# Kernel tuning notes

Measured on AMD Instinct MI355X. Metric: run time of the kernel, lower is better.

The kernel has to match this reference:

```python
import jax, jax.numpy as jnp
import numpy as np

N_NODES = 100000
N_EDGES = 3200000
IN_CH = 128
HID = 64
OUT_CH = 2
BN_EPS = 1e-5


def setup_inputs() -> dict:
    key = jax.random.key(0)
    ks = jax.random.split(key, 16)
    def glorot(k, shape):
        fan_in, fan_out = shape[0], shape[1]
        lim = jnp.sqrt(6.0 / (fan_in + fan_out))
        return jax.random.uniform(k, shape, jnp.float32, -lim, lim)
    inp = {
        "x": jax.random.normal(ks[0], (N_NODES, IN_CH), jnp.float32),
        "edge_index": jax.random.randint(ks[1], (2, N_EDGES), 0, N_NODES, jnp.int64),
        # input projection + input BN
        "Wp": glorot(ks[2], (IN_CH, HID)),
        "bp": jnp.zeros((HID,), jnp.float32),
        "g_in": jnp.ones((HID,), jnp.float32),
        "b_in": jnp.zeros((HID,), jnp.float32),
        # SAGEConv layer 0: lin_l (aggr, with bias) + lin_r (self, no bias)
        "Wl0": glorot(ks[3], (HID, HID)),
        "bl0": jnp.zeros((HID,), jnp.float32),
        "Wr0": glorot(ks[4], (HID, HID)),
        "g0": jnp.ones((HID,), jnp.float32),
        "b0": jnp.zeros((HID,), jnp.float32),
        # SAGEConv layer 1
        "Wl1": glorot(ks[5], (HID, HID)),
        "bl1": jnp.zeros((HID,), jnp.float32),
        "Wr1": glorot(ks[6], (HID, HID)),
        "g1": jnp.ones((HID,), jnp.float32),
        "b1": jnp.zeros((HID,), jnp.float32),
        # output head
        "Wo": glorot(ks[7], (HID, OUT_CH)),
        "bo": jnp.zeros((OUT_CH,), jnp.float32),
    }
    return inp


def _bn(h, g, b):
    # training-mode batchnorm over node dim (biased variance, as torch)
    m = h.mean(axis=0)
    v = h.var(axis=0)
    return g * (h - m) * jax.lax.rsqrt(v + BN_EPS) + b


def _sage_conv(h, src, dst, Wl, bl, Wr):
    # mean aggregation of source features at destination nodes
    msg = h[src]                                              # [E, HID]
    summed = jax.ops.segment_sum(msg, dst, num_segments=N_NODES)
    cnt = jax.ops.segment_sum(jnp.ones((src.shape[0],), h.dtype), dst,
                              num_segments=N_NODES)
    aggr = summed / jnp.maximum(cnt, 1.0)[:, None]
    return aggr @ Wl + bl + h @ Wr


def reference(x, edge_index, Wp, bp, g_in, b_in,
              Wl0, bl0, Wr0, g0, b0,
              Wl1, bl1, Wr1, g1, b1,
              Wo, bo):
    src, dst = edge_index[0], edge_index[1]
    h = jax.nn.relu(_bn(x @ Wp + bp, g_in, b_in))   # dropout: eval no-op
    h_prev = h
    # layer 0 (i=0: no residual)
    h_new = jax.nn.relu(_bn(_sage_conv(h, src, dst, Wl0, bl0, Wr0), g0, b0))
    h_prev, h = h, h_new
    # layer 1 (i=1: residual with h_prev)
    h_new = jax.nn.relu(_bn(_sage_conv(h, src, dst, Wl1, bl1, Wr1), g1, b1))
    h_new = h_new + h_prev
    h = h_new
    return h @ Wo + bo
```

## Files before the change

kernel.cpp:

```cpp
#include <hip/hip_runtime.h>
#include <hip/hip_bf16.h>

#define NN 100000
#define NE 3200000
#define IC 128
#define HD 64
#define BN_EPS 1e-5f
#define NBUK 196
#define MSB 16

__device__ __forceinline__ float bf2f(unsigned short u) {
  return __uint_as_float(((unsigned)u) << 16);
}
__device__ __forceinline__ unsigned int f2bf(float f) {
  unsigned int u = __float_as_uint(f);
  return (u + 0x7FFFu + ((u >> 16) & 1u)) >> 16;
}

__global__ __launch_bounds__(256) void k_gemm_in(
    const float* __restrict__ x, const float* __restrict__ Wp,
    const float* __restrict__ bp, float* __restrict__ pre,
    float* __restrict__ stats) {
  __shared__ float sW[IC * HD];
  __shared__ float sX[64 * 130];
  __shared__ float ssS[1024], ssQ[1024];
  int tid = threadIdx.x;
  for (int i = tid; i < IC * HD / 4; i += 256)
    *(float4*)&sW[i * 4] = *(const float4*)&Wp[i * 4];
  int cg = tid & 15, rg = tid >> 4;
  int c0 = cg * 4;
  float4 bpc = *(const float4*)&bp[c0];
  float S[4] = {0.f, 0.f, 0.f, 0.f}, Q[4] = {0.f, 0.f, 0.f, 0.f};
  const int NT = (NN + 63) / 64;
  for (int t = blockIdx.x; t < NT; t += gridDim.x) {
    int row0 = t * 64;
    __syncthreads();
    for (int i = tid; i < 64 * IC / 4; i += 256) {
      int r = i >> 5, k4 = i & 31;
      int grow = row0 + r;
      if (grow >= NN) grow = NN - 1;
      *(float4*)&sX[r * 130 + k4 * 4] =
          *(const float4*)&x[(size_t)grow * IC + k4 * 4];
    }
    __syncthreads();
    float acc[4][4];
#pragma unroll
    for (int r = 0; r < 4; ++r)
#pragma unroll
      for (int c = 0; c < 4; ++c) acc[r][c] = ((const float*)&bpc)[c];
    for (int kg = 0; kg < IC; kg += 4) {
      float4 xr[4], wv[4];
#pragma unroll
      for (int r = 0; r < 4; ++r)
        xr[r] = *(const float4*)&sX[(rg * 4 + r) * 130 + kg];
#pragma unroll
      for (int j = 0; j < 4; ++j)
        wv[j] = *(const float4*)&sW[(kg + j) * HD + c0];
#pragma unroll
      for (int j = 0; j < 4; ++j)
#pragma unroll
        for (int r = 0; r < 4; ++r) {
          float xv = ((const float*)&xr[r])[j];
          acc[r][0] = fmaf(xv, ((const float*)&wv[j])[0], acc[r][0]);
          acc[r][1] = fmaf(xv, ((const float*)&wv[j])[1], acc[r][1]);
          acc[r][2] = fmaf(xv, ((const float*)&wv[j])[2], acc[r][2]);
          acc[r][3] = fmaf(xv, ((const float*)&wv[j])[3], acc[r][3]);
        }
    }
#pragma unroll
    for (int r = 0; r < 4; ++r) {
      int row = row0 + rg * 4 + r;
      if (row < NN) {
        *(float4*)&pre[(size_t)row * HD + c0] = *(float4*)&acc[r][0];
#pragma unroll
        for (int c = 0; c < 4; ++c) {
          S[c] += acc[r][c];
          Q[c] = fmaf(acc[r][c], acc[r][c], Q[c]);
        }
      }
    }
  }
#pragma unroll
  for (int c = 0; c < 4; ++c) {
    ssS[tid * 4 + c] = S[c];
    ssQ[tid * 4 + c] = Q[c];
  }
  __syncthreads();
  if (tid < 64) {
    int cgr = tid >> 2, cc = tid & 3;
    float Ts = 0.f, Tq = 0.f;
#pragma unroll
    for (int m = 0; m < 16; ++m) {
      Ts += ssS[(m * 16 + cgr) * 4 + cc];
      Tq += ssQ[(m * 16 + cgr) * 4 + cc];
    }
    atomicAdd(&stats[tid], Ts);
    atomicAdd(&stats[64 + tid], Tq);
  }
}

__global__ __launch_bounds__(256) void k_bn_relu(
    const float* __restrict__ pre, const float* __restrict__ stats,
    const float* __restrict__ g, const float* __restrict__ b,
    __hip_bfloat16* __restrict__ out16) {
  size_t i = (size_t)blockIdx.x * 256 + threadIdx.x;
  int c = threadIdx.x & 63;
  const float invN = 1.0f / NN;
  float m = stats[c] * invN;
  float v = stats[64 + c] * invN - m * m;
  float sc = g[c] * rsqrtf(v + BN_EPS);
  float val = (pre[i] - m) * sc + b[c];
  out16[i] = __float2bfloat16(fmaxf(val, 0.f));
}

__global__ __launch_bounds__(256) void k_bhist(
    const int* __restrict__ dst, unsigned int* __restrict__ bcnt) {
  __shared__ unsigned int h[NBUK];
  for (int i = threadIdx.x; i < NBUK; i += 256) h[i] = 0u;
  __syncthreads();
  int i0 = blockIdx.x * 256 + threadIdx.x;
  int stride = gridDim.x * 256;
  for (int e = i0; e < NE; e += stride)
    atomicAdd(&h[((unsigned)dst[e]) >> 9], 1u);
  __syncthreads();
  for (int i = threadIdx.x; i < NBUK; i += 256)
    if (h[i]) atomicAdd(&bcnt[i], h[i]);
}

__global__ __launch_bounds__(256) void k_bscan(
    const unsigned int* __restrict__ bcnt, unsigned int* __restrict__ gstart,
    unsigned int* __restrict__ gcur) {
  __shared__ unsigned int s[256];
  int t = threadIdx.x;
  unsigned int my = (t < NBUK) ? bcnt[t] : 0u;
  s[t] = my;
  __syncthreads();
  for (int off = 1; off < 256; off <<= 1) {
    unsigned int v = (t >= off) ? s[t - off] : 0u;
    __syncthreads();
    s[t] += v;
    __syncthreads();
  }
  if (t < NBUK) {
    gstart[t] = s[t] - my;
    gcur[t] = s[t] - my;
  }
  if (t == NBUK - 1) gstart[NBUK] = s[t];
}

__global__ __launch_bounds__(256) void k_msplit(
    const int* __restrict__ src, const int* __restrict__ dst,
    unsigned int* __restrict__ gcur, unsigned int* __restrict__ staging) {
  __shared__ unsigned int hist[NBUK];
  __shared__ unsigned int gbase[NBUK];
  int tid = threadIdx.x;
  for (int i = tid; i < NBUK; i += 256) hist[i] = 0u;
  __syncthreads();
  int e0 = blockIdx.x * (256 * MSB);
  unsigned int pk[MSB], rk[MSB], bk[MSB];
#pragma unroll
  for (int i = 0; i < MSB; ++i) {
    int e = e0 + i * 256 + tid;
    if (e < NE) {
      int d = dst[e];
      unsigned int b = (unsigned int)(d >> 9);
      rk[i] = atomicAdd(&hist[b], 1u);
      pk[i] = (unsigned int)src[e] | ((unsigned int)(d & 511) << 17);
      bk[i] = b;
    } else {
      bk[i] = 0xFFFFFFFFu;
    }
  }
  __syncthreads();
  for (int i = tid; i < NBUK; i += 256)
    if (hist[i]) gbase[i] = atomicAdd(&gcur[i], hist[i]);
  __syncthreads();
#pragma unroll
  for (int i = 0; i < MSB; ++i)
    if (bk[i] != 0xFFFFFFFFu) staging[gbase[bk[i]] + rk[i]] = pk[i];
}

__global__ __launch_bounds__(512) void k_bucket_sort(
    const unsigned int* __restrict__ staging,
    const unsigned int* __restrict__ gstart, unsigned int* __restrict__ nstart,
    unsigned int* __restrict__ srcoff) {
  __shared__ unsigned int hist[512];
  __shared__ unsigned int sc[512];
  __shared__ unsigned int cur[512];
  int b = blockIdx.x, t = threadIdx.x;
  hist[t] = 0u;
  __syncthreads();
  int lo = (int)gstart[b], hi = (int)gstart[b + 1];
  for (int e = lo + t; e < hi; e += 512)
    atomicAdd(&hist[staging[e] >> 17], 1u);
  __syncthreads();
  unsigned int my = hist[t];
  sc[t] = my;
  __syncthreads();
  for (int off = 1; off < 512; off <<= 1) {
    unsigned int v = (t >= off) ? sc[t - off] : 0u;
    __syncthreads();
    sc[t] += v;
    __syncthreads();
  }
  unsigned int st = (unsigned int)lo + sc[t] - my;
  cur[t] = st;
  int node = b * 512 + t;
  if (node < NN) {
    nstart[node] = st;
    if (node == NN - 1) nstart[NN] = st + my;
  }
  __syncthreads();
  for (int e = lo + t; e < hi; e += 512) {
    unsigned int u = staging[e];
    unsigned int pos = atomicAdd(&cur[u >> 17], 1u);
    srcoff[pos] = (u & 0x1FFFFu) << 7;
  }
}

__global__ __launch_bounds__(256) void k_aggr_sorted(
    const unsigned int* __restrict__ srcoff,
    const unsigned int* __restrict__ nstart,
    const unsigned short* __restrict__ h16,
    unsigned short* __restrict__ a16) {
  int lane = threadIdx.x & 63;
  int n = (int)((blockIdx.x * 256 + threadIdx.x) >> 6);
  if (n >= NN) return;
  int g = lane >> 3;
  int q = lane & 7;
  int e0 = (int)nstart[n];
  int e1 = (int)nstart[n + 1];
  const char* hbase = (const char*)h16 + q * 16;
  float a0 = 0.f, a1 = 0.f, a2 = 0.f, a3 = 0.f;
  float a4 = 0.f, a5 = 0.f, a6 = 0.f, a7 = 0.f;
  float b0 = 0.f, b1 = 0.f, b2 = 0.f, b3 = 0.f;
  float b4 = 0.f, b5 = 0.f, b6 = 0.f, b7 = 0.f;
  int e = e0 + g;
  for (; e + 8 < e1; e += 16) {
    unsigned int o0 = srcoff[e];
    unsigned int o1 = srcoff[e + 8];
    uint4 u0 = *(const uint4*)(hbase + o0);
    uint4 u1 = *(const uint4*)(hbase + o1);
    a0 += __uint_as_float(u0.x << 16);
    a1 += __uint_as_float(u0.x & 0xFFFF0000u);
    a2 += __uint_as_float(u0.y << 16);
    a3 += __uint_as_float(u0.y & 0xFFFF0000u);
    a4 += __uint_as_float(u0.z << 16);
    a5 += __uint_as_float(u0.z & 0xFFFF0000u);
    a6 += __uint_as_float(u0.w << 16);
    a7 += __uint_as_float(u0.w & 0xFFFF0000u);
    b0 += __uint_as_float(u1.x << 16);
    b1 += __uint_as_float(u1.x & 0xFFFF0000u);
    b2 += __uint_as_float(u1.y << 16);
    b3 += __uint_as_float(u1.y & 0xFFFF0000u);
    b4 += __uint_as_float(u1.z << 16);
    b5 += __uint_as_float(u1.z & 0xFFFF0000u);
    b6 += __uint_as_float(u1.w << 16);
    b7 += __uint_as_float(u1.w & 0xFFFF0000u);
  }
  if (e < e1) {
    unsigned int o0 = srcoff[e];
    uint4 u0 = *(const uint4*)(hbase + o0);
    a0 += __uint_as_float(u0.x << 16);
    a1 += __uint_as_float(u0.x & 0xFFFF0000u);
    a2 += __uint_as_float(u0.y << 16);
    a3 += __uint_as_float(u0.y & 0xFFFF0000u);
    a4 += __uint_as_float(u0.z << 16);
    a5 += __uint_as_float(u0.z & 0xFFFF0000u);
    a6 += __uint_as_float(u0.w << 16);
    a7 += __uint_as_float(u0.w & 0xFFFF0000u);
  }
  a0 += b0; a1 += b1; a2 += b2; a3 += b3;
  a4 += b4; a5 += b5; a6 += b6; a7 += b7;
#pragma unroll
  for (int off = 8; off <= 32; off <<= 1) {
    a0 += __shfl_xor(a0, off);
    a1 += __shfl_xor(a1, off);
    a2 += __shfl_xor(a2, off);
    a3 += __shfl_xor(a3, off);
    a4 += __shfl_xor(a4, off);
    a5 += __shfl_xor(a5, off);
    a6 += __shfl_xor(a6, off);
    a7 += __shfl_xor(a7, off);
  }
  if (g == 0) {
    float cntf = (float)(e1 - e0);
    float inv = (cntf > 0.f) ? 1.0f / cntf : 0.f;
    uint4 o;
    o.x = f2bf(a0 * inv) | (f2bf(a1 * inv) << 16);
    o.y = f2bf(a2 * inv) | (f2bf(a3 * inv) << 16);
    o.z = f2bf(a4 * inv) | (f2bf(a5 * inv) << 16);
    o.w = f2bf(a6 * inv) | (f2bf(a7 * inv) << 16);
    *(uint4*)((char*)a16 + (size_t)n * 128 + q * 16) = o;
  }
}

__global__ __launch_bounds__(256) void k_combine(
    const unsigned short* __restrict__ a16,
    const unsigned short* __restrict__ h16, const float* __restrict__ Wl,
    const float* __restrict__ bl, const float* __restrict__ Wr,
    float* __restrict__ pre, float* __restrict__ stats) {
  __shared__ float sWl[HD * HD], sWr[HD * HD];
  __shared__ float sA[64 * 66], sH[64 * 66];
  __shared__ float ssS[1024], ssQ[1024];
  int tid = threadIdx.x;
  for (int i = tid; i < HD * HD / 4; i += 256) {
    *(float4*)&sWl[i * 4] = *(const float4*)&Wl[i * 4];
    *(float4*)&sWr[i * 4] = *(const float4*)&Wr[i * 4];
  }
  int cg = tid & 15, rg = tid >> 4;
  int c0 = cg * 4;
  float4 blc = *(const float4*)&bl[c0];
  float S[4] = {0.f, 0.f, 0.f, 0.f}, Q[4] = {0.f, 0.f, 0.f, 0.f};
  const int NT = (NN + 63) / 64;
  for (int t = blockIdx.x; t < NT; t += gridDim.x) {
    int row0 = t * 64;
    __syncthreads();
    for (int i = tid; i < 1024; i += 256) {
      int r = i >> 4, k4 = i & 15;
      int grow = row0 + r;
      if (grow >= NN) grow = NN - 1;
      uint2 au = *(const uint2*)&a16[(size_t)grow * HD + k4 * 4];
      float* dA = &sA[r * 66 + k4 * 4];
      dA[0] = bf2f((unsigned short)(au.x & 0xFFFFu));
      dA[1] = bf2f((unsigned short)(au.x >> 16));
      dA[2] = bf2f((unsigned short)(au.y & 0xFFFFu));
      dA[3] = bf2f((unsigned short)(au.y >> 16));
      uint2 hu = *(const uint2*)&h16[(size_t)grow * HD + k4 * 4];
      float* dH = &sH[r * 66 + k4 * 4];
      dH[0] = bf2f((unsigned short)(hu.x & 0xFFFFu));
      dH[1] = bf2f((unsigned short)(hu.x >> 16));
      dH[2] = bf2f((unsigned short)(hu.y & 0xFFFFu));
      dH[3] = bf2f((unsigned short)(hu.y >> 16));
    }
    __syncthreads();
    float acc[4][4];
#pragma unroll
    for (int r = 0; r < 4; ++r)
#pragma unroll
      for (int c = 0; c < 4; ++c) acc[r][c] = ((const float*)&blc)[c];
    for (int kg = 0; kg < HD; kg += 4) {
      float4 ar[4], hr[4], wlv[4], wrv[4];
#pragma unroll
      for (int r = 0; r < 4; ++r) {
        ar[r] = *(const float4*)&sA[(rg * 4 + r) * 66 + kg];
        hr[r] = *(const float4*)&sH[(rg * 4 + r) * 66 + kg];
      }
#pragma unroll
      for (int j = 0; j < 4; ++j) {
        wlv[j] = *(const float4*)&sWl[(kg + j) * HD + c0];
        wrv[j] = *(const float4*)&sWr[(kg + j) * HD + c0];
      }
#pragma unroll
      for (int j = 0; j < 4; ++j)
#pragma unroll
        for (int r = 0; r < 4; ++r) {
          float av = ((const float*)&ar[r])[j];
          float hv = ((const float*)&hr[r])[j];
#pragma unroll
          for (int c = 0; c < 4; ++c) {
            acc[r][c] = fmaf(av, ((const float*)&wlv[j])[c], acc[r][c]);
            acc[r][c] = fmaf(hv, ((const float*)&wrv[j])[c], acc[r][c]);
          }
        }
    }
#pragma unroll
    for (int r = 0; r < 4; ++r) {
      int row = row0 + rg * 4 + r;
      if (row < NN) {
        *(float4*)&pre[(size_t)row * HD + c0] = *(float4*)&acc[r][0];
#pragma unroll
        for (int c = 0; c < 4; ++c) {
          S[c] += acc[r][c];
          Q[c] = fmaf(acc[r][c], acc[r][c], Q[c]);
        }
      }
    }
  }
#pragma unroll
  for (int c = 0; c < 4; ++c) {
    ssS[tid * 4 + c] = S[c];
    ssQ[tid * 4 + c] = Q[c];
  }
  __syncthreads();
  if (tid < 64) {
    int cgr = tid >> 2, cc = tid & 3;
    float Ts = 0.f, Tq = 0.f;
#pragma unroll
    for (int m = 0; m < 16; ++m) {
      Ts += ssS[(m * 16 + cgr) * 4 + cc];
      Tq += ssQ[(m * 16 + cgr) * 4 + cc];
    }
    atomicAdd(&stats[tid], Ts);
    atomicAdd(&stats[64 + tid], Tq);
  }
}

__global__ __launch_bounds__(256) void k_bn_relu_head(
    const float* __restrict__ pre, const float* __restrict__ stats,
    const float* __restrict__ g, const float* __restrict__ b,
    const unsigned short* __restrict__ resid16, const float* __restrict__ Wo,
    const float* __restrict__ bo, float* __restrict__ out) {
  int lane = threadIdx.x & 63;
  int wid = (int)((blockIdx.x * blockDim.x + threadIdx.x) >> 6);
  int nw = (int)((gridDim.x * blockDim.x) >> 6);
  const float invN = 1.0f / NN;
  float m = stats[lane] * invN;
  float v = stats[64 + lane] * invN - m * m;
  float sc = g[lane] * rsqrtf(v + BN_EPS);
  float bb = b[lane];
  float w0 = Wo[lane * 2], w1 = Wo[lane * 2 + 1];
  float b0 = bo[0], b1 = bo[1];
  for (int row = wid; row < NN; row += nw) {
    size_t i = (size_t)row * HD + lane;
    float val = (pre[i] - m) * sc + bb;
    val = fmaxf(val, 0.f) + bf2f(resid16[i]);
    float a0 = val * w0, a1 = val * w1;
#pragma unroll
    for (int off = 32; off > 0; off >>= 1) {
      a0 += __shfl_down(a0, off);
      a1 += __shfl_down(a1, off);
    }
    if (lane == 0) {
      out[(size_t)row * 2] = a0 + b0;
      out[(size_t)row * 2 + 1] = a1 + b1;
    }
  }
}

extern "C" void kernel_launch(void* const* d_in, const int* in_sizes, int n_in,
                              void* d_out, int out_size, void* d_ws,
                              size_t ws_size, hipStream_t stream) {
  const float* x = (const float*)d_in[0];
  const int* ei = (const int*)d_in[1];
  const float* Wp = (const float*)d_in[2];
  const float* bp = (const float*)d_in[3];
  const float* g_in = (const float*)d_in[4];
  const float* b_in = (const float*)d_in[5];
  const float* Wl0 = (const float*)d_in[6];
  const float* bl0 = (const float*)d_in[7];
  const float* Wr0 = (const float*)d_in[8];
  const float* g0 = (const float*)d_in[9];
  const float* b0 = (const float*)d_in[10];
  const float* Wl1 = (const float*)d_in[11];
  const float* bl1 = (const float*)d_in[12];
  const float* Wr1 = (const float*)d_in[13];
  const float* g1 = (const float*)d_in[14];
  const float* b1 = (const float*)d_in[15];
  const float* Wo = (const float*)d_in[16];
  const float* bo = (const float*)d_in[17];
  float* out = (float*)d_out;

  const int* src = ei;
  const int* dst = ei + NE;

  float* ws = (float*)d_ws;
  float* pre = ws;
  __hip_bfloat16* h0b = (__hip_bfloat16*)(ws + (size_t)NN * HD);
  __hip_bfloat16* h1b = h0b + (size_t)NN * HD;
  unsigned short* a16 = (unsigned short*)(h1b + (size_t)NN * HD);
  unsigned int* staging = (unsigned int*)(a16 + (size_t)NN * HD);
  unsigned int* srcoff = staging + NE;
  unsigned int* nstart = srcoff + NE;
  unsigned int* bcnt = nstart + NN + 1;
  unsigned int* gstart = bcnt + NBUK;
  unsigned int* gcur = gstart + NBUK + 1;
  float* stats0 = (float*)(gcur + NBUK);
  float* stats1 = stats0 + 128;
  float* stats2 = stats1 + 128;

  const int ELEM_BLOCKS = (NN * HD) / 256;
  const int AGGR_BLOCKS = 25000;
  const int MS_BLOCKS = (NE + 256 * MSB - 1) / (256 * MSB);

  hipMemsetAsync(stats0, 0, 3 * 128 * sizeof(float), stream);
  hipMemsetAsync(bcnt, 0, NBUK * sizeof(unsigned int), stream);

  k_gemm_in<<<512, 256, 0, stream>>>(x, Wp, bp, pre, stats0);
  k_bn_relu<<<ELEM_BLOCKS, 256, 0, stream>>>(pre, stats0, g_in, b_in, h0b);

  k_bhist<<<1024, 256, 0, stream>>>(dst, bcnt);
  k_bscan<<<1, 256, 0, stream>>>(bcnt, gstart, gcur);
  k_msplit<<<MS_BLOCKS, 256, 0, stream>>>(src, dst, gcur, staging);
  k_bucket_sort<<<NBUK, 512, 0, stream>>>(staging, gstart, nstart, srcoff);

  k_aggr_sorted<<<AGGR_BLOCKS, 256, 0, stream>>>(
      srcoff, nstart, (const unsigned short*)h0b, a16);
  k_combine<<<512, 256, 0, stream>>>(a16, (const unsigned short*)h0b, Wl0,
                                     bl0, Wr0, pre, stats1);
  k_bn_relu<<<ELEM_BLOCKS, 256, 0, stream>>>(pre, stats1, g0, b0, h1b);

  k_aggr_sorted<<<AGGR_BLOCKS, 256, 0, stream>>>(
      srcoff, nstart, (const unsigned short*)h1b, a16);
  k_combine<<<512, 256, 0, stream>>>(a16, (const unsigned short*)h1b, Wl1,
                                     bl1, Wr1, pre, stats2);
  k_bn_relu_head<<<1024, 256, 0, stream>>>(pre, stats2, g1, b1,
                                           (const unsigned short*)h0b, Wo, bo,
                                           out);
}
```

Baseline: 399.8 us.

## Store pre-BN activations and staged tiles in bf16, shuffle-reduce BN stats

Pre-batchnorm activations are now written and read as packed bf16 instead of fp32, which halves the traffic between the GEMM kernels and the BN kernels. The input x tile and the aggregation and self tiles are staged in LDS as packed bf16 and unpacked in registers, cutting shared-memory footprint so more blocks can be resident. BN statistics are reduced with wave shuffles instead of a large LDS array, k_bn_relu processes four elements per thread, and the GEMM grids grow from 512 to 768 blocks. This adds rounding error to x and to the pre-BN values, and costs extra unpack work in the inner loops.

```diff
diff --git a/kernel.cpp b/kernel.cpp
--- a/kernel.cpp
+++ b/kernel.cpp
@@ -16,14 +16,17 @@
   unsigned int u = __float_as_uint(f);
   return (u + 0x7FFFu + ((u >> 16) & 1u)) >> 16;
 }
+__device__ __forceinline__ unsigned int pack2(float a, float b) {
+  return f2bf(a) | (f2bf(b) << 16);
+}
 
 __global__ __launch_bounds__(256) void k_gemm_in(
     const float* __restrict__ x, const float* __restrict__ Wp,
-    const float* __restrict__ bp, float* __restrict__ pre,
+    const float* __restrict__ bp, unsigned int* __restrict__ pre16,
     float* __restrict__ stats) {
   __shared__ float sW[IC * HD];
-  __shared__ float sX[64 * 130];
-  __shared__ float ssS[1024], ssQ[1024];
+  __shared__ unsigned int sXu[64 * 68];
+  __shared__ float sStS[256], sStQ[256];
   int tid = threadIdx.x;
   for (int i = tid; i < IC * HD / 4; i += 256)
     *(float4*)&sW[i * 4] = *(const float4*)&Wp[i * 4];
@@ -35,12 +38,19 @@
   for (int t = blockIdx.x; t < NT; t += gridDim.x) {
     int row0 = t * 64;
     __syncthreads();
-    for (int i = tid; i < 64 * IC / 4; i += 256) {
-      int r = i >> 5, k4 = i & 31;
+    for (int i = tid; i < 1024; i += 256) {
+      int r = i >> 4, k8 = i & 15;
       int grow = row0 + r;
       if (grow >= NN) grow = NN - 1;
-      *(float4*)&sX[r * 130 + k4 * 4] =
-          *(const float4*)&x[(size_t)grow * IC + k4 * 4];
+      const float* xs = &x[(size_t)grow * IC + k8 * 8];
+      float4 f0 = *(const float4*)xs;
+      float4 f1 = *(const float4*)(xs + 4);
+      uint4 p;
+      p.x = pack2(f0.x, f0.y);
+      p.y = pack2(f0.z, f0.w);
+      p.z = pack2(f1.x, f1.y);
+      p.w = pack2(f1.z, f1.w);
+      *(uint4*)&sXu[r * 68 + k8 * 4] = p;
     }
     __syncthreads();
     float acc[4][4];
@@ -49,29 +59,37 @@
 #pragma unroll
       for (int c = 0; c < 4; ++c) acc[r][c] = ((const float*)&bpc)[c];
     for (int kg = 0; kg < IC; kg += 4) {
-      float4 xr[4], wv[4];
+      uint2 xu[4];
+      float4 wv[4];
 #pragma unroll
       for (int r = 0; r < 4; ++r)
-        xr[r] = *(const float4*)&sX[(rg * 4 + r) * 130 + kg];
+        xu[r] = *(const uint2*)&sXu[(rg * 4 + r) * 68 + (kg >> 1)];
 #pragma unroll
       for (int j = 0; j < 4; ++j)
         wv[j] = *(const float4*)&sW[(kg + j) * HD + c0];
 #pragma unroll
-      for (int j = 0; j < 4; ++j)
-#pragma unroll
-        for (int r = 0; r < 4; ++r) {
-          float xv = ((const float*)&xr[r])[j];
-          acc[r][0] = fmaf(xv, ((const float*)&wv[j])[0], acc[r][0]);
-          acc[r][1] = fmaf(xv, ((const float*)&wv[j])[1], acc[r][1]);
-          acc[r][2] = fmaf(xv, ((const float*)&wv[j])[2], acc[r][2]);
-          acc[r][3] = fmaf(xv, ((const float*)&wv[j])[3], acc[r][3]);
+      for (int r = 0; r < 4; ++r) {
+        float xv[4];
+        xv[0] = __uint_as_float(xu[r].x << 16);
+        xv[1] = __uint_as_float(xu[r].x & 0xFFFF0000u);
+        xv[2] = __uint_as_float(xu[r].y << 16);
+        xv[3] = __uint_as_float(xu[r].y & 0xFFFF0000u);
+#pragma unroll
+        for (int j = 0; j < 4; ++j) {
+#pragma unroll
+          for (int c = 0; c < 4; ++c)
+            acc[r][c] = fmaf(xv[j], ((const float*)&wv[j])[c], acc[r][c]);
         }
+      }
     }
 #pragma unroll
     for (int r = 0; r < 4; ++r) {
       int row = row0 + rg * 4 + r;
       if (row < NN) {
-        *(float4*)&pre[(size_t)row * HD + c0] = *(float4*)&acc[r][0];
+        uint2 o;
+        o.x = pack2(acc[r][0], acc[r][1]);
+        o.y = pack2(acc[r][2], acc[r][3]);
+        *(uint2*)&pre16[(size_t)row * 32 + cg * 2] = o;
 #pragma unroll
         for (int c = 0; c < 4; ++c) {
           S[c] += acc[r][c];
@@ -82,35 +100,52 @@
   }
 #pragma unroll
   for (int c = 0; c < 4; ++c) {
-    ssS[tid * 4 + c] = S[c];
-    ssQ[tid * 4 + c] = Q[c];
+    S[c] += __shfl_xor(S[c], 16);
+    S[c] += __shfl_xor(S[c], 32);
+    Q[c] += __shfl_xor(Q[c], 16);
+    Q[c] += __shfl_xor(Q[c], 32);
+  }
+  int wave = tid >> 6, lane = tid & 63;
+  if (lane < 16) {
+#pragma unroll
+    for (int c = 0; c < 4; ++c) {
+      sStS[wave * 64 + lane * 4 + c] = S[c];
+      sStQ[wave * 64 + lane * 4 + c] = Q[c];
+    }
   }
   __syncthreads();
   if (tid < 64) {
-    int cgr = tid >> 2, cc = tid & 3;
-    float Ts = 0.f, Tq = 0.f;
-#pragma unroll
-    for (int m = 0; m < 16; ++m) {
-      Ts += ssS[(m * 16 + cgr) * 4 + cc];
-      Tq += ssQ[(m * 16 + cgr) * 4 + cc];
-    }
+    float Ts = sStS[tid] + sStS[64 + tid] + sStS[128 + tid] + sStS[192 + tid];
+    float Tq = sStQ[tid] + sStQ[64 + tid] + sStQ[128 + tid] + sStQ[192 + tid];
     atomicAdd(&stats[tid], Ts);
     atomicAdd(&stats[64 + tid], Tq);
   }
 }
 
 __global__ __launch_bounds__(256) void k_bn_relu(
-    const float* __restrict__ pre, const float* __restrict__ stats,
+    const unsigned int* __restrict__ pre16, const float* __restrict__ stats,
     const float* __restrict__ g, const float* __restrict__ b,
-    __hip_bfloat16* __restrict__ out16) {
+    unsigned int* __restrict__ h16u) {
   size_t i = (size_t)blockIdx.x * 256 + threadIdx.x;
-  int c = threadIdx.x & 63;
+  int c0 = ((int)(i & 15)) * 4;
   const float invN = 1.0f / NN;
-  float m = stats[c] * invN;
-  float v = stats[64 + c] * invN - m * m;
-  float sc = g[c] * rsqrtf(v + BN_EPS);
-  float val = (pre[i] - m) * sc + b[c];
-  out16[i] = __float2bfloat16(fmaxf(val, 0.f));
+  uint2 p = *(const uint2*)&pre16[i * 2];
+  float v[4];
+  v[0] = __uint_as_float(p.x << 16);
+  v[1] = __uint_as_float(p.x & 0xFFFF0000u);
+  v[2] = __uint_as_float(p.y << 16);
+  v[3] = __uint_as_float(p.y & 0xFFFF0000u);
+#pragma unroll
+  for (int c = 0; c < 4; ++c) {
+    float m = stats[c0 + c] * invN;
+    float var = stats[64 + c0 + c] * invN - m * m;
+    float sc = g[c0 + c] * rsqrtf(var + BN_EPS);
+    v[c] = fmaxf((v[c] - m) * sc + b[c0 + c], 0.f);
+  }
+  uint2 o;
+  o.x = pack2(v[0], v[1]);
+  o.y = pack2(v[2], v[3]);
+  *(uint2*)&h16u[i * 2] = o;
 }
 
 __global__ __launch_bounds__(256) void k_bhist(
@@ -287,22 +322,22 @@
     float cntf = (float)(e1 - e0);
     float inv = (cntf > 0.f) ? 1.0f / cntf : 0.f;
     uint4 o;
-    o.x = f2bf(a0 * inv) | (f2bf(a1 * inv) << 16);
-    o.y = f2bf(a2 * inv) | (f2bf(a3 * inv) << 16);
-    o.z = f2bf(a4 * inv) | (f2bf(a5 * inv) << 16);
-    o.w = f2bf(a6 * inv) | (f2bf(a7 * inv) << 16);
+    o.x = pack2(a0 * inv, a1 * inv);
+    o.y = pack2(a2 * inv, a3 * inv);
+    o.z = pack2(a4 * inv, a5 * inv);
+    o.w = pack2(a6 * inv, a7 * inv);
     *(uint4*)((char*)a16 + (size_t)n * 128 + q * 16) = o;
   }
 }
 
 __global__ __launch_bounds__(256) void k_combine(
-    const unsigned short* __restrict__ a16,
-    const unsigned short* __restrict__ h16, const float* __restrict__ Wl,
+    const unsigned int* __restrict__ a16u,
+    const unsigned int* __restrict__ h16u, const float* __restrict__ Wl,
     const float* __restrict__ bl, const float* __restrict__ Wr,
-    float* __restrict__ pre, float* __restrict__ stats) {
+    unsigned int* __restrict__ pre16, float* __restrict__ stats) {
   __shared__ float sWl[HD * HD], sWr[HD * HD];
-  __shared__ float sA[64 * 66], sH[64 * 66];
-  __shared__ float ssS[1024], ssQ[1024];
+  __shared__ unsigned int sAu[64 * 36], sHu[64 * 36];
+  __shared__ float sStS[256], sStQ[256];
   int tid = threadIdx.x;
   for (int i = tid; i < HD * HD / 4; i += 256) {
     *(float4*)&sWl[i * 4] = *(const float4*)&Wl[i * 4];
@@ -316,22 +351,14 @@
   for (int t = blockIdx.x; t < NT; t += gridDim.x) {
     int row0 = t * 64;
     __syncthreads();
-    for (int i = tid; i < 1024; i += 256) {
-      int r = i >> 4, k4 = i & 15;
+    for (int i = tid; i < 512; i += 256) {
+      int r = i >> 3, c4 = i & 7;
       int grow = row0 + r;
       if (grow >= NN) grow = NN - 1;
-      uint2 au = *(const uint2*)&a16[(size_t)grow * HD + k4 * 4];
-      float* dA = &sA[r * 66 + k4 * 4];
-      dA[0] = bf2f((unsigned short)(au.x & 0xFFFFu));
-      dA[1] = bf2f((unsigned short)(au.x >> 16));
-      dA[2] = bf2f((unsigned short)(au.y & 0xFFFFu));
-      dA[3] = bf2f((unsigned short)(au.y >> 16));
-      uint2 hu = *(const uint2*)&h16[(size_t)grow * HD + k4 * 4];
-      float* dH = &sH[r * 66 + k4 * 4];
-      dH[0] = bf2f((unsigned short)(hu.x & 0xFFFFu));
-      dH[1] = bf2f((unsigned short)(hu.x >> 16));
-      dH[2] = bf2f((unsigned short)(hu.y & 0xFFFFu));
-      dH[3] = bf2f((unsigned short)(hu.y >> 16));
+      *(uint4*)&sAu[r * 36 + c4 * 4] =
+          *(const uint4*)&a16u[(size_t)grow * 32 + c4 * 4];
+      *(uint4*)&sHu[r * 36 + c4 * 4] =
+          *(const uint4*)&h16u[(size_t)grow * 32 + c4 * 4];
     }
     __syncthreads();
     float acc[4][4];
@@ -340,11 +367,12 @@
 #pragma unroll
       for (int c = 0; c < 4; ++c) acc[r][c] = ((const float*)&blc)[c];
     for (int kg = 0; kg < HD; kg += 4) {
-      float4 ar[4], hr[4], wlv[4], wrv[4];
+      uint2 au[4], hu[4];
+      float4 wlv[4], wrv[4];
 #pragma unroll
       for (int r = 0; r < 4; ++r) {
-        ar[r] = *(const float4*)&sA[(rg * 4 + r) * 66 + kg];
-        hr[r] = *(const float4*)&sH[(rg * 4 + r) * 66 + kg];
+        au[r] = *(const uint2*)&sAu[(rg * 4 + r) * 36 + (kg >> 1)];
+        hu[r] = *(const uint2*)&sHu[(rg * 4 + r) * 36 + (kg >> 1)];
       }
 #pragma unroll
       for (int j = 0; j < 4; ++j) {
@@ -352,23 +380,34 @@
         wrv[j] = *(const float4*)&sWr[(kg + j) * HD + c0];
       }
 #pragma unroll
-      for (int j = 0; j < 4; ++j)
-#pragma unroll
-        for (int r = 0; r < 4; ++r) {
-          float av = ((const float*)&ar[r])[j];
-          float hv = ((const float*)&hr[r])[j];
+      for (int r = 0; r < 4; ++r) {
+        float av[4], hv[4];
+        av[0] = __uint_as_float(au[r].x << 16);
+        av[1] = __uint_as_float(au[r].x & 0xFFFF0000u);
+        av[2] = __uint_as_float(au[r].y << 16);
+        av[3] = __uint_as_float(au[r].y & 0xFFFF0000u);
+        hv[0] = __uint_as_float(hu[r].x << 16);
+        hv[1] = __uint_as_float(hu[r].x & 0xFFFF0000u);
+        hv[2] = __uint_as_float(hu[r].y << 16);
+        hv[3] = __uint_as_float(hu[r].y & 0xFFFF0000u);
+#pragma unroll
+        for (int j = 0; j < 4; ++j) {
 #pragma unroll
           for (int c = 0; c < 4; ++c) {
-            acc[r][c] = fmaf(av, ((const float*)&wlv[j])[c], acc[r][c]);
-            acc[r][c] = fmaf(hv, ((const float*)&wrv[j])[c], acc[r][c]);
+            acc[r][c] = fmaf(av[j], ((const float*)&wlv[j])[c], acc[r][c]);
+            acc[r][c] = fmaf(hv[j], ((const float*)&wrv[j])[c], acc[r][c]);
           }
         }
+      }
     }
 #pragma unroll
     for (int r = 0; r < 4; ++r) {
       int row = row0 + rg * 4 + r;
       if (row < NN) {
-        *(float4*)&pre[(size_t)row * HD + c0] = *(float4*)&acc[r][0];
+        uint2 o;
+        o.x = pack2(acc[r][0], acc[r][1]);
+        o.y = pack2(acc[r][2], acc[r][3]);
+        *(uint2*)&pre16[(size_t)row * 32 + cg * 2] = o;
 #pragma unroll
         for (int c = 0; c < 4; ++c) {
           S[c] += acc[r][c];
@@ -379,28 +418,34 @@
   }
 #pragma unroll
   for (int c = 0; c < 4; ++c) {
-    ssS[tid * 4 + c] = S[c];
-    ssQ[tid * 4 + c] = Q[c];
+    S[c] += __shfl_xor(S[c], 16);
+    S[c] += __shfl_xor(S[c], 32);
+    Q[c] += __shfl_xor(Q[c], 16);
+    Q[c] += __shfl_xor(Q[c], 32);
+  }
+  int wave = tid >> 6, lane = tid & 63;
+  if (lane < 16) {
+#pragma unroll
+    for (int c = 0; c < 4; ++c) {
+      sStS[wave * 64 + lane * 4 + c] = S[c];
+      sStQ[wave * 64 + lane * 4 + c] = Q[c];
+    }
   }
   __syncthreads();
   if (tid < 64) {
-    int cgr = tid >> 2, cc = tid & 3;
-    float Ts = 0.f, Tq = 0.f;
-#pragma unroll
-    for (int m = 0; m < 16; ++m) {
-      Ts += ssS[(m * 16 + cgr) * 4 + cc];
-      Tq += ssQ[(m * 16 + cgr) * 4 + cc];
-    }
+    float Ts = sStS[tid] + sStS[64 + tid] + sStS[128 + tid] + sStS[192 + tid];
+    float Tq = sStQ[tid] + sStQ[64 + tid] + sStQ[128 + tid] + sStQ[192 + tid];
     atomicAdd(&stats[tid], Ts);
     atomicAdd(&stats[64 + tid], Tq);
   }
 }
 
 __global__ __launch_bounds__(256) void k_bn_relu_head(
-    const float* __restrict__ pre, const float* __restrict__ stats,
-    const float* __restrict__ g, const float* __restrict__ b,
-    const unsigned short* __restrict__ resid16, const float* __restrict__ Wo,
-    const float* __restrict__ bo, float* __restrict__ out) {
+    const unsigned short* __restrict__ pre16,
+    const float* __restrict__ stats, const float* __restrict__ g,
+    const float* __restrict__ b, const unsigned short* __restrict__ resid16,
+    const float* __restrict__ Wo, const float* __restrict__ bo,
+    float* __restrict__ out) {
   int lane = threadIdx.x & 63;
   int wid = (int)((blockIdx.x * blockDim.x + threadIdx.x) >> 6);
   int nw = (int)((gridDim.x * blockDim.x) >> 6);
@@ -413,7 +458,7 @@
   float b0 = bo[0], b1 = bo[1];
   for (int row = wid; row < NN; row += nw) {
     size_t i = (size_t)row * HD + lane;
-    float val = (pre[i] - m) * sc + bb;
+    float val = (bf2f(pre16[i]) - m) * sc + bb;
     val = fmaxf(val, 0.f) + bf2f(resid16[i]);
     float a0 = val * w0, a1 = val * w1;
 #pragma unroll
@@ -454,11 +499,10 @@
   const int* src = ei;
   const int* dst = ei + NE;
 
-  float* ws = (float*)d_ws;
-  float* pre = ws;
-  __hip_bfloat16* h0b = (__hip_bfloat16*)(ws + (size_t)NN * HD);
-  __hip_bfloat16* h1b = h0b + (size_t)NN * HD;
-  unsigned short* a16 = (unsigned short*)(h1b + (size_t)NN * HD);
+  unsigned int* pre16 = (unsigned int*)d_ws;
+  unsigned short* h0 = (unsigned short*)(pre16 + (size_t)NN * 32);
+  unsigned short* h1 = h0 + (size_t)NN * HD;
+  unsigned short* a16 = h1 + (size_t)NN * HD;
   unsigned int* staging = (unsigned int*)(a16 + (size_t)NN * HD);
   unsigned int* srcoff = staging + NE;
   unsigned int* nstart = srcoff + NE;
@@ -469,32 +513,33 @@
   float* stats1 = stats0 + 128;
   float* stats2 = stats1 + 128;
 
-  const int ELEM_BLOCKS = (NN * HD) / 256;
+  const int BNR_BLOCKS = (NN * HD / 4) / 256;
   const int AGGR_BLOCKS = 25000;
   const int MS_BLOCKS = (NE + 256 * MSB - 1) / (256 * MSB);
 
   hipMemsetAsync(stats0, 0, 3 * 128 * sizeof(float), stream);
   hipMemsetAsync(bcnt, 0, NBUK * sizeof(unsigned int), stream);
 
-  k_gemm_in<<<512, 256, 0, stream>>>(x, Wp, bp, pre, stats0);
-  k_bn_relu<<<ELEM_BLOCKS, 256, 0, stream>>>(pre, stats0, g_in, b_in, h0b);
+  k_gemm_in<<<768, 256, 0, stream>>>(x, Wp, bp, pre16, stats0);
+  k_bn_relu<<<BNR_BLOCKS, 256, 0, stream>>>(pre16, stats0, g_in, b_in,
+                                            (unsigned int*)h0);
 
   k_bhist<<<1024, 256, 0, stream>>>(dst, bcnt);
   k_bscan<<<1, 256, 0, stream>>>(bcnt, gstart, gcur);
   k_msplit<<<MS_BLOCKS, 256, 0, stream>>>(src, dst, gcur, staging);
   k_bucket_sort<<<NBUK, 512, 0, stream>>>(staging, gstart, nstart, srcoff);
 
-  k_aggr_sorted<<<AGGR_BLOCKS, 256, 0, stream>>>(
-      srcoff, nstart, (const unsigned short*)h0b, a16);
-  k_combine<<<512, 256, 0, stream>>>(a16, (const unsigned short*)h0b, Wl0,
-                                     bl0, Wr0, pre, stats1);
-  k_bn_relu<<<ELEM_BLOCKS, 256, 0, stream>>>(pre, stats1, g0, b0, h1b);
-
-  k_aggr_sorted<<<AGGR_BLOCKS, 256, 0, stream>>>(
-      srcoff, nstart, (const unsigned short*)h1b, a16);
-  k_combine<<<512, 256, 0, stream>>>(a16, (const unsigned short*)h1b, Wl1,
-                                     bl1, Wr1, pre, stats2);
-  k_bn_relu_head<<<1024, 256, 0, stream>>>(pre, stats2, g1, b1,
-                                           (const unsigned short*)h0b, Wo, bo,
-                                           out);
-}
+  k_aggr_sorted<<<AGGR_BLOCKS, 256, 0, stream>>>(srcoff, nstart, h0, a16);
+  k_combine<<<768, 256, 0, stream>>>((const unsigned int*)a16,
+                                     (const unsigned int*)h0, Wl0, bl0, Wr0,
+                                     pre16, stats1);
+  k_bn_relu<<<BNR_BLOCKS, 256, 0, stream>>>(pre16, stats1, g0, b0,
+                                            (unsigned int*)h1);
+
+  k_aggr_sorted<<<AGGR_BLOCKS, 256, 0, stream>>>(srcoff, nstart, h1, a16);
+  k_combine<<<768, 256, 0, stream>>>((const unsigned int*)a16,
+                                     (const unsigned int*)h1, Wl1, bl1, Wr1,
+                                     pre16, stats2);
+  k_bn_relu_head<<<1024, 256, 0, stream>>>((const unsigned short*)pre16,
+                                           stats2, g1, b1, h0, Wo, bo, out);
+}
```

Result: no change. 395.8 us (-1.0%).
